# Optimization experiments

Hardware: AMD Instinct MI355X
Metric: run time of the kernel (lower is better)

Reference implementation:

```python
import jax, jax.numpy as jnp
import numpy as np

B, I, H = 8192, 1024, 1024

def setup_inputs() -> dict:
    key = jax.random.key(0)
    ks = jax.random.split(key, 5)
    # xavier-uniform-ish scale for weights
    sW = float(np.sqrt(6.0 / (I + H)))
    sU = float(np.sqrt(6.0 / (H + H)))
    return {
        "x": jax.random.normal(ks[0], (B, I), jnp.float32),
        "h": jax.random.normal(ks[1], (B, H), jnp.float32),
        "c": jax.random.normal(ks[2], (B, H), jnp.float32),
        # gate order along leading axis: 0=i, 1=f, 2=o, 3=c_hat
        "W": jax.random.uniform(ks[3], (4, H, I), jnp.float32, -sW, sW),
        "bW": jnp.zeros((4, H), jnp.float32),
        "U": jax.random.uniform(ks[4], (4, H, H), jnp.float32, -sU, sU),
        "bU": jnp.zeros((4, H), jnp.float32),
    }

def reference(x, h, c, W, bW, U, bU):
    # two batched GEMMs covering all 8 original Linear layers
    gx = jnp.einsum('bi,ghi->gbh', x, W) + bW[:, None, :]   # [4,B,H]
    gh = jnp.einsum('bk,ghk->gbh', h, U) + bU[:, None, :]   # [4,B,H]
    g = gx + gh
    i = jax.nn.sigmoid(g[0])
    f = jax.nn.sigmoid(g[1])
    o = jax.nn.sigmoid(g[2])
    c_hat = jnp.tanh(g[3])
    c_new = f * c + i * c_hat
    h_new = o * jnp.tanh(c_new)
    return (h_new, (h_new, c_new))
```

## Files before the change

### kernel.cpp

```cpp
#include <hip/hip_runtime.h>
#include <hip/hip_bf16.h>

typedef __hip_bfloat16 bf16;
typedef __attribute__((ext_vector_type(8))) short short8;
typedef __attribute__((ext_vector_type(4))) float floatx4;

#define B_DIM 8192
#define H_DIM 1024
#define KSUM 2048
#define BM 256
#define BN 256
#define BK 64
#define KT 32
#define NSLOT 10
#define SLOT_ELEMS 8192
#define CEX_STRIDE 68

union BS { bf16 b; short s; };
__device__ __forceinline__ short cvt1(float f) {
  BS u; u.b = __float2bfloat16(f); return u.s;
}
__device__ __forceinline__ short8 cvt8(float4 lo, float4 hi) {
  short8 r;
  r[0] = cvt1(lo.x); r[1] = cvt1(lo.y); r[2] = cvt1(lo.z); r[3] = cvt1(lo.w);
  r[4] = cvt1(hi.x); r[5] = cvt1(hi.y); r[6] = cvt1(hi.z); r[7] = cvt1(hi.w);
  return r;
}

__device__ __forceinline__ void async_ld16(const bf16* g, bf16* lds) {
  __builtin_amdgcn_global_load_lds(
      (const __attribute__((address_space(1))) unsigned int*)g,
      (__attribute__((address_space(3))) unsigned int*)lds,
      16, 0, 0);
}

__global__ __launch_bounds__(256) void cvt_pack(
    const float* __restrict__ x, const float* __restrict__ h,
    const float* __restrict__ W, const float* __restrict__ U,
    bf16* __restrict__ Ac, bf16* __restrict__ Bc) {
  const int blk = blockIdx.x;
  if (blk < 8192) {
    const int idx = blk * 256 + threadIdx.x;
    const long row = idx >> 8;
    const int k0 = (idx & 255) << 3;
    const float* src = (k0 < 1024) ? (x + row * 1024 + k0)
                                   : (h + row * 1024 + (k0 - 1024));
    const float4 lo = *(const float4*)src;
    const float4 hi = *(const float4*)(src + 4);
    *(short8*)(Ac + row * KSUM + k0) = cvt8(lo, hi);
  } else {
    const int idx = (blk - 8192) * 256 + threadIdx.x;
    const long r = idx >> 8;
    const int k0 = (idx & 255) << 3;
    const int g = (int)(r & 3);
    const long hh = r >> 2;
    const long base = (long)g * (H_DIM * H_DIM) + hh * H_DIM;
    const float* src = (k0 < 1024) ? (W + base + k0) : (U + base + (k0 - 1024));
    const float4 lo = *(const float4*)src;
    const float4 hi = *(const float4*)(src + 4);
    *(short8*)(Bc + r * KSUM + k0) = cvt8(lo, hi);
  }
}

__device__ __forceinline__ float sigmoidf_(float v) {
  return 1.0f / (1.0f + __expf(-v));
}
__device__ __forceinline__ float tanhf_(float v) {
  return 1.0f - 2.0f / (__expf(2.0f * v) + 1.0f);
}
__device__ __forceinline__ float getc(const float4& v, int t) {
  return t == 0 ? v.x : t == 1 ? v.y : t == 2 ? v.z : v.w;
}

__global__ __launch_bounds__(512, 2) void gemm_lstm(
    const bf16* __restrict__ Ac, const bf16* __restrict__ Bc,
    const float* __restrict__ cprev_g, const float* __restrict__ bW,
    const float* __restrict__ bU, float* __restrict__ out) {
  extern __shared__ __align__(16) char smem[];
  bf16* const ring = (bf16*)smem;
  float* const cex = (float*)smem;

  const int tid  = threadIdx.x;
  const int lane = tid & 63;
  const int wv   = tid >> 6;
  const int wm_idx = wv >> 2;
  const int wn_idx = wv & 3;

  const int blk  = blockIdx.x;
  const int xcd  = blk & 7;
  const int slot = blk >> 3;
  const int mt   = slot & 31;
  const int nt   = (xcd << 1) | (slot >> 5);
  const long m0 = (long)mt * BM;
  const long n0 = (long)nt * BN;

  const int lrow   = lane >> 3;
  const int lchunk = lane & 7;
  const int schunk = lchunk ^ lrow;
  const bf16* const aRow0 = Ac + (m0 + wv * 8 + lrow) * (long)KSUM + schunk * 8;
  const bf16* const bRow0 = Bc + (n0 + wv * 8 + lrow) * (long)KSUM + schunk * 8;

  const int col16 = lane & 15;
  const int quad  = lane >> 4;
  const int x7    = col16 & 7;
  const int bRowOff = (wn_idx & 1) << 6;

  floatx4 acc[8][4];
#pragma unroll
  for (int i = 0; i < 8; ++i)
#pragma unroll
    for (int jq = 0; jq < 4; ++jq) acc[i][jq] = (floatx4){0.f, 0.f, 0.f, 0.f};

#define STAGE_HALF(h_)                                                        \
  {                                                                           \
    const int c_ = (h_) & 3;                                                  \
    const long off_ = ((long)((c_ >> 1) * 128)) * KSUM + (long)(((h_) >> 2) * BK); \
    const bf16* s_ = ((c_ & 1) ? bRow0 : aRow0) + off_;                       \
    bf16* d_ = ring + ((h_) % NSLOT) * SLOT_ELEMS + wv * 512;                 \
    async_ld16(s_, d_);                                                       \
    async_ld16(s_ + 64L * KSUM, d_ + 4096);                                   \
  }

#define STAGE_P(p_)                                                           \
  { const int h_ = 4 * j + (p_) + 6; if (h_ < 4 * KT) STAGE_HALF(h_); }

#define RD_A(dst, rh_, s_)                                                    \
  _Pragma("unroll") for (int fi = 0; fi < 4; ++fi)                            \
    dst[fi] = *(const short8*)&rA[((rh_) * 64 + fi * 16 + col16) * 64 +       \
                                  (((((s_) << 2) + quad) ^ x7) << 3)];

#define RD_B(dst, s_)                                                         \
  _Pragma("unroll") for (int fj = 0; fj < 4; ++fj)                            \
    dst[fj] = *(const short8*)&rB[(bRowOff + fj * 16 + col16) * 64 +          \
                                  (((((s_) << 2) + quad) ^ x7) << 3)];

#define MM(accrow_, a_, b_)                                                   \
  __builtin_amdgcn_s_setprio(1);                                              \
  _Pragma("unroll") for (int fi = 0; fi < 4; ++fi)                            \
    _Pragma("unroll") for (int fj = 0; fj < 4; ++fj)                          \
      acc[(accrow_) + fi][fj] = __builtin_amdgcn_mfma_f32_16x16x32_bf16(      \
          a_[fi], b_[fj], acc[(accrow_) + fi][fj], 0, 0, 0);                  \
  __builtin_amdgcn_s_setprio(0);

#define FENCE() __builtin_amdgcn_sched_barrier(0)

#pragma unroll
  for (int h = 0; h < 6; ++h) STAGE_HALF(h);
  asm volatile("s_waitcnt vmcnt(4)" ::: "memory");
  __builtin_amdgcn_s_barrier();

#pragma unroll 1
  for (int j = 0; j < KT; ++j) {
    const bf16* const rA =
        ring + ((4 * j + 2 * wm_idx) % NSLOT) * SLOT_ELEMS;
    const bf16* const rB =
        ring + ((4 * j + 1 + ((wn_idx >> 1) << 1)) % NSLOT) * SLOT_ELEMS;
    short8 a0s0[4], a0s1[4], a1s0[4], a1s1[4], b_s0[4], b_s1[4];

    RD_A(a0s0, 0, 0) RD_B(b_s0, 0)
    FENCE();
    RD_A(a0s1, 0, 1) RD_B(b_s1, 1)
    FENCE();
    STAGE_P(0) STAGE_P(1)
    FENCE();
    MM(0, a0s0, b_s0)
    FENCE();
    RD_A(a1s0, 1, 0)
    FENCE();
    MM(0, a0s1, b_s1)
    FENCE();
    RD_A(a1s1, 1, 1)
    STAGE_P(2) STAGE_P(3)
    FENCE();
    MM(4, a1s0, b_s0)
    MM(4, a1s1, b_s1)
    if (j < KT - 2) asm volatile("s_waitcnt vmcnt(4)" ::: "memory");
    else            asm volatile("s_waitcnt vmcnt(0)" ::: "memory");
    __builtin_amdgcn_s_barrier();
  }

  const int rquad = (lane >> 4) << 2;
  const int row16 = lane & 15;
  const int tq    = lane >> 4;
  const long hglob = ((n0 + (long)(wn_idx << 6)) >> 2) + tq * 4;

  float4 bsum[4];
#pragma unroll
  for (int g = 0; g < 4; ++g) {
    const float4 a = *(const float4*)(bW + g * H_DIM + hglob);
    const float4 b = *(const float4*)(bU + g * H_DIM + hglob);
    bsum[g] = (float4){a.x + b.x, a.y + b.y, a.z + b.z, a.w + b.w};
  }

  float* wx = cex + wv * (16 * CEX_STRIDE);
  const long BH = (long)B_DIM * H_DIM;

#pragma unroll
  for (int ig = 0; ig < 8; ++ig) {
#pragma unroll
    for (int jj = 0; jj < 4; ++jj)
#pragma unroll
      for (int r = 0; r < 4; ++r)
        wx[(rquad + r) * CEX_STRIDE + jj * 16 + col16] = acc[ig][jj][r];

    float4 g4[4];
#pragma unroll
    for (int t = 0; t < 4; ++t)
      g4[t] = *(const float4*)&wx[row16 * CEX_STRIDE + (tq * 4 + t) * 4];

    const long mrow = m0 + (long)wm_idx * 128 + ig * 16 + row16;
    const float4 cp4 = *(const float4*)(cprev_g + mrow * H_DIM + hglob);

    float hn[4], cn[4];
#pragma unroll
    for (int t = 0; t < 4; ++t) {
      const float gi = g4[t].x + getc(bsum[0], t);
      const float gf = g4[t].y + getc(bsum[1], t);
      const float go = g4[t].z + getc(bsum[2], t);
      const float gg = g4[t].w + getc(bsum[3], t);
      const float I = sigmoidf_(gi);
      const float F = sigmoidf_(gf);
      const float O = sigmoidf_(go);
      const float G = tanhf_(gg);
      const float cv = F * getc(cp4, t) + I * G;
      hn[t] = O * tanhf_(cv);
      cn[t] = cv;
    }
    const float4 hn4 = {hn[0], hn[1], hn[2], hn[3]};
    const float4 cn4 = {cn[0], cn[1], cn[2], cn[3]};
    const long ob = mrow * H_DIM + hglob;
    *(float4*)(out + ob)          = hn4;
    *(float4*)(out + BH + ob)     = hn4;
    *(float4*)(out + 2 * BH + ob) = cn4;
  }
}

extern "C" void kernel_launch(void* const* d_in, const int* in_sizes, int n_in,
                              void* d_out, int out_size, void* d_ws, size_t ws_size,
                              hipStream_t stream) {
  const float* x  = (const float*)d_in[0];
  const float* h  = (const float*)d_in[1];
  const float* c  = (const float*)d_in[2];
  const float* W  = (const float*)d_in[3];
  const float* bW = (const float*)d_in[4];
  const float* U  = (const float*)d_in[5];
  const float* bU = (const float*)d_in[6];
  float* out = (float*)d_out;

  bf16* Ac = (bf16*)d_ws;
  bf16* Bc = (bf16*)((char*)d_ws + (size_t)33554432);

  static bool attr_done = false;
  if (!attr_done) {
    hipFuncSetAttribute(reinterpret_cast<const void*>(gemm_lstm),
                        hipFuncAttributeMaxDynamicSharedMemorySize, 163840);
    attr_done = true;
  }

  cvt_pack<<<12288, 256, 0, stream>>>(x, h, W, U, Ac, Bc);
  gemm_lstm<<<512, 512, 163840, stream>>>(Ac, Bc, c, bW, bU, out);
}
```

Baseline: 337.2 us.

## Restructure K-loop into four barrier-synchronized LDS-read/MFMA phases

Reorders the per-iteration schedule into four phases. Each phase issues LDS fragment reads and one async global stage, then a workgroup barrier and lgkmcnt wait, then a 16-MFMA block, then another barrier. The intent is to keep waves in lockstep so LDS reads and MFMA bursts from different waves interleave better, ping-pong style. The cost is many more barriers per iteration and stalls on full LDS waits before each MFMA block.

Result: slower. 344.7 us (+2.2%).

```diff
diff --git a/kernel.cpp b/kernel.cpp
--- a/kernel.cpp
+++ b/kernel.cpp
@@ -124,17 +124,23 @@
 #define STAGE_P(p_)                                                           \
   { const int h_ = 4 * j + (p_) + 6; if (h_ < 4 * KT) STAGE_HALF(h_); }
 
-#define RD_A(dst, rh_, s_)                                                    \
+#define RD_A4(dst, rh_, s_)                                                   \
   _Pragma("unroll") for (int fi = 0; fi < 4; ++fi)                            \
     dst[fi] = *(const short8*)&rA[((rh_) * 64 + fi * 16 + col16) * 64 +       \
                                   (((((s_) << 2) + quad) ^ x7) << 3)];
 
-#define RD_B(dst, s_)                                                         \
+#define RD_B4(dst, s_)                                                        \
   _Pragma("unroll") for (int fj = 0; fj < 4; ++fj)                            \
     dst[fj] = *(const short8*)&rB[(bRowOff + fj * 16 + col16) * 64 +          \
                                   (((((s_) << 2) + quad) ^ x7) << 3)];
 
-#define MM(accrow_, a_, b_)                                                   \
+#define SYNC()                                                                \
+  __builtin_amdgcn_sched_barrier(0);                                          \
+  __builtin_amdgcn_s_barrier();                                               \
+  asm volatile("s_waitcnt lgkmcnt(0)" ::: "memory");                          \
+  __builtin_amdgcn_sched_barrier(0);
+
+#define MM16(accrow_, a_, b_)                                                 \
   __builtin_amdgcn_s_setprio(1);                                              \
   _Pragma("unroll") for (int fi = 0; fi < 4; ++fi)                            \
     _Pragma("unroll") for (int fj = 0; fj < 4; ++fj)                          \
@@ -142,8 +148,6 @@
           a_[fi], b_[fj], acc[(accrow_) + fi][fj], 0, 0, 0);                  \
   __builtin_amdgcn_s_setprio(0);
 
-#define FENCE() __builtin_amdgcn_sched_barrier(0)
-
 #pragma unroll
   for (int h = 0; h < 6; ++h) STAGE_HALF(h);
   asm volatile("s_waitcnt vmcnt(4)" ::: "memory");
@@ -155,27 +159,33 @@
         ring + ((4 * j + 2 * wm_idx) % NSLOT) * SLOT_ELEMS;
     const bf16* const rB =
         ring + ((4 * j + 1 + ((wn_idx >> 1) << 1)) % NSLOT) * SLOT_ELEMS;
-    short8 a0s0[4], a0s1[4], a1s0[4], a1s1[4], b_s0[4], b_s1[4];
-
-    RD_A(a0s0, 0, 0) RD_B(b_s0, 0)
-    FENCE();
-    RD_A(a0s1, 0, 1) RD_B(b_s1, 1)
-    FENCE();
-    STAGE_P(0) STAGE_P(1)
-    FENCE();
-    MM(0, a0s0, b_s0)
-    FENCE();
-    RD_A(a1s0, 1, 0)
-    FENCE();
-    MM(0, a0s1, b_s1)
-    FENCE();
-    RD_A(a1s1, 1, 1)
-    STAGE_P(2) STAGE_P(3)
-    FENCE();
-    MM(4, a1s0, b_s0)
-    MM(4, a1s1, b_s1)
+    short8 af0s0[4], af0s1[4], af1s0[4], af1s1[4], bf_s0[4], bf_s1[4];
+
+    RD_A4(af0s0, 0, 0) RD_B4(bf_s0, 0)
+    STAGE_P(0)
+    SYNC()
+    MM16(0, af0s0, bf_s0)
+    __builtin_amdgcn_s_barrier();
+
+    RD_A4(af0s1, 0, 1) RD_B4(bf_s1, 1)
+    STAGE_P(1)
+    SYNC()
+    MM16(0, af0s1, bf_s1)
+    __builtin_amdgcn_s_barrier();
+
+    RD_A4(af1s0, 1, 0)
+    STAGE_P(2)
+    SYNC()
+    MM16(4, af1s0, bf_s0)
+    __builtin_amdgcn_s_barrier();
+
+    RD_A4(af1s1, 1, 1)
+    STAGE_P(3)
+    __builtin_amdgcn_sched_barrier(0);
     if (j < KT - 2) asm volatile("s_waitcnt vmcnt(4)" ::: "memory");
     else            asm volatile("s_waitcnt vmcnt(0)" ::: "memory");
+    SYNC()
+    MM16(4, af1s1, bf_s1)
     __builtin_amdgcn_s_barrier();
   }
 
```
